# Kernel optimization log

Measured on AMD Instinct MI355X. Metric: run time of the kernel, lower is better.

## Reference

```python
import jax, jax.numpy as jnp
import numpy as np

NUM_BINS = 8
C_OUT = 64
CA_RED = 8  # channel-attention reduction (CBAM default-style)


def _bn(x, g, b):
    # BatchNorm1d in training mode: batch statistics, eps=1e-3
    mu = x.mean(0)
    var = x.var(0)
    return (x - mu) / jnp.sqrt(var + 1e-3) * g + b


def setup_inputs() -> dict:
    key = jax.random.key(0)
    ks = jax.random.split(key, 20)
    Nv, U = 400000, 200000
    s = 0.05
    inp = {
        'voxel_features': jax.random.normal(ks[0], (Nv, 5), jnp.float32),
        'voxel_features_coords': jax.random.randint(ks[1], (Nv, 4), 0, NUM_BINS),
        'v_feat_unq_coords': jax.random.randint(ks[2], (U,), 0, 1000000),
        'v_feat_unq_inv': jax.random.randint(ks[3], (Nv,), 0, U),
        'v_feat_unq_cnt': jax.random.randint(ks[4], (U,), 0, 5),
        # up_dimension: Linear(5,32)+ReLU, Linear(32,64)
        'up_w1': jax.random.normal(ks[5], (5, C_OUT // 2), jnp.float32) * s,
        'up_b1': jnp.zeros((C_OUT // 2,), jnp.float32),
        'up_w2': jax.random.normal(ks[6], (C_OUT // 2, C_OUT), jnp.float32) * s,
        'up_b2': jnp.zeros((C_OUT,), jnp.float32),
        # ZBAM (CBAM-1d): channel-attention shared MLP + spatial conv k=7
        'ca_w1': jax.random.normal(ks[7], (C_OUT, C_OUT // CA_RED), jnp.float32) * s,
        'ca_w2': jax.random.normal(ks[8], (C_OUT // CA_RED, C_OUT), jnp.float32) * s,
        'sa_conv': jax.random.normal(ks[9], (1, 2, 7), jnp.float32) * s,  # OIH
        # bin_shuffle: Linear(512,256,no bias)+BN+ReLU, Linear(256,64,no bias)+BN+ReLU
        'bs_w1': jax.random.normal(ks[10], (C_OUT * NUM_BINS, C_OUT * NUM_BINS // 2), jnp.float32) * s,
        'bn1_g': jnp.ones((C_OUT * NUM_BINS // 2,), jnp.float32),
        'bn1_b': jnp.zeros((C_OUT * NUM_BINS // 2,), jnp.float32),
        'bs_w2': jax.random.normal(ks[11], (C_OUT * NUM_BINS // 2, C_OUT), jnp.float32) * s,
        'bn2_g': jnp.ones((C_OUT,), jnp.float32),
        'bn2_b': jnp.zeros((C_OUT,), jnp.float32),
    }
    return inp


def reference(voxel_features, voxel_features_coords, v_feat_unq_coords,
              v_feat_unq_inv, v_feat_unq_cnt,
              up_w1, up_b1, up_w2, up_b2,
              ca_w1, ca_w2, sa_conv,
              bs_w1, bn1_g, bn1_b, bs_w2, bn2_g, bn2_b):
    coords = voxel_features_coords
    U = v_feat_unq_coords.shape[0]
    binz = coords[:, 1]
    # --- binning: scatter voxels into (pillar, z-bin) slots ---
    src = jnp.zeros((U, NUM_BINS, 6), jnp.float32)
    src = src.at[v_feat_unq_inv, binz, 1:].set(voxel_features)
    src = src.at[:, :, 0].set(-1.0)
    src = src.at[v_feat_unq_inv, binz, 0].set(coords[:, 0].astype(jnp.float32))
    # --- occupancy mask + compaction (eager nonzero) ---
    idx = jnp.nonzero(v_feat_unq_cnt >= 2)[0]
    src = src[idx]                      # (N, P=8, 6)
    feat = src[:, :, 1:]                # (N, 8, 5)
    # --- up_dimension MLP ---
    h = jnp.maximum(feat @ up_w1 + up_b1, 0.0) @ up_w2 + up_b2  # (N, 8, 64)
    x = jnp.swapaxes(h, 1, 2)           # (N, C=64, P=8)
    # --- ZBAM: CBAM-style channel + spatial attention over z-bins ---
    def ca_mlp(v):
        return jnp.maximum(v @ ca_w1, 0.0) @ ca_w2
    ca = jax.nn.sigmoid(ca_mlp(x.mean(-1)) + ca_mlp(x.max(-1)))  # (N, C)
    x = x * ca[:, :, None]
    sa_in = jnp.stack([x.mean(1), x.max(1)], axis=1)             # (N, 2, P)
    sa = jax.lax.conv_general_dilated(sa_in, sa_conv, (1,), [(3, 3)],
                                      dimension_numbers=('NCH', 'OIH', 'NCH'))
    x = x * jax.nn.sigmoid(sa)          # (N, C, P)
    # --- bin_shuffle: flatten (C,P) row-major as torch .view does ---
    flat = x.reshape(x.shape[0], C_OUT * NUM_BINS)  # (N, 512)
    y = jnp.maximum(_bn(flat @ bs_w1, bn1_g, bn1_b), 0.0)
    y = jnp.maximum(_bn(y @ bs_w2, bn2_g, bn2_b), 0.0)
    return y
```

## Files before the change

kernel.cpp:

```cpp
#include <hip/hip_runtime.h>
#include <cmath>

typedef __attribute__((ext_vector_type(8))) short short8;
typedef __attribute__((ext_vector_type(4))) float f32x4;

__device__ __forceinline__ ushort f2b(float x) {
    union { float f; unsigned u; } v; v.f = x;
    unsigned r = v.u + 0x7FFFu + ((v.u >> 16) & 1u);
    return (ushort)(r >> 16);
}
__device__ __forceinline__ float b2f(ushort h) {
    union { unsigned u; float f; } v; v.u = ((unsigned)h) << 16; return v.f;
}
__device__ __forceinline__ float sigm(float x) { return 1.0f / (1.0f + __expf(-x)); }

template <int C>
__device__ __forceinline__ float dppf(float x) {
    return __builtin_bit_cast(float,
        __builtin_amdgcn_update_dpp(0, __builtin_bit_cast(int, x), C, 0xf, 0xf, true));
}
__device__ __forceinline__ float rsum16(float v) {
    v += dppf<0x140>(v);
    v += dppf<0x141>(v);
    v += dppf<0x1B>(v);
    v += dppf<0xB1>(v);
    return v;
}
__device__ __forceinline__ float rmax16(float v) {
    v = fmaxf(v, dppf<0x140>(v));
    v = fmaxf(v, dppf<0x141>(v));
    v = fmaxf(v, dppf<0x1B>(v));
    v = fmaxf(v, dppf<0xB1>(v));
    return v;
}
__device__ __forceinline__ float swzf16(float x) {
    return __builtin_bit_cast(float,
        __builtin_amdgcn_ds_swizzle(__builtin_bit_cast(int, x), 0x401F));
}
__device__ __forceinline__ unsigned swzu16(unsigned x) {
    return (unsigned)__builtin_amdgcn_ds_swizzle((int)x, 0x401F);
}

#define GL16(g, s) __builtin_amdgcn_global_load_lds( \
    (const __attribute__((address_space(1))) unsigned int*)(g), \
    (__attribute__((address_space(3))) unsigned int*)(s), 16, 0, 0)

__global__ void k_scatter_winner(const int* __restrict__ inv,
                                 const int* __restrict__ coords,
                                 int Nv, int* __restrict__ winner) {
    int v = blockIdx.x * 256 + threadIdx.x;
    if (v < Nv) {
        int u = inv[v];
        int b = coords[v * 4 + 1];
        atomicMax(&winner[u * 8 + b], v);
    }
}

__global__ void k_count(const int* __restrict__ cnt, int U, int* __restrict__ bc) {
    int i = blockIdx.x * 256 + threadIdx.x;
    int s = (i < U && cnt[i] >= 2) ? 1 : 0;
    unsigned long long m = __ballot(s);
    __shared__ int wc[4];
    int lane = threadIdx.x & 63, w = threadIdx.x >> 6;
    if (lane == 0) wc[w] = __popcll(m);
    __syncthreads();
    if (threadIdx.x == 0) bc[blockIdx.x] = wc[0] + wc[1] + wc[2] + wc[3];
}

__global__ void k_scan_wave(int* __restrict__ d, int n) {
    int l = threadIdx.x;
    int carry = 0;
    for (int base = 0; base < n; base += 64) {
        int v = (base + l < n) ? d[base + l] : 0;
        int s = v;
        #pragma unroll
        for (int o = 1; o < 64; o <<= 1) {
            int q = __shfl_up(s, o);
            if (l >= o) s += q;
        }
        if (base + l < n) d[base + l] = carry + s - v;
        carry += __shfl(s, 63);
    }
}

__global__ void k_write_sel(const int* __restrict__ cnt, int U,
                            const int* __restrict__ boff, int* __restrict__ sel) {
    int i = blockIdx.x * 256 + threadIdx.x;
    int s = (i < U && cnt[i] >= 2) ? 1 : 0;
    unsigned long long m = __ballot(s);
    __shared__ int wc[4];
    int lane = threadIdx.x & 63, w = threadIdx.x >> 6;
    if (lane == 0) wc[w] = __popcll(m);
    __syncthreads();
    int off = boff[blockIdx.x];
    for (int j = 0; j < w; j++) off += wc[j];
    if (s) sel[off + __popcll(m & ((1ull << lane) - 1ull))] = i;
}

__global__ void k_prep_w(const float* __restrict__ w1, const float* __restrict__ w2,
                         ushort* __restrict__ w1t, ushort* __restrict__ w2t) {
    int i = blockIdx.x * 256 + threadIdx.x;
    if (i < 512 * 256) {
        int n = i >> 9, k = i & 511;
        w1t[i] = f2b(w1[k * 256 + n]);
    }
    int j = i - 512 * 256;
    if (j >= 0 && j < 256 * 64) {
        int n = j >> 8, k = j & 255;
        w2t[j] = f2b(w2[k * 64 + n]);
    }
}

__global__ __launch_bounds__(64) void k_feat4(
    const float* __restrict__ vf, const int* __restrict__ winner,
    const int* __restrict__ sel,
    const float* __restrict__ up_w1, const float* __restrict__ up_b1,
    const float* __restrict__ up_w2, const float* __restrict__ up_b2,
    const float* __restrict__ ca_w1, const float* __restrict__ ca_w2,
    const float* __restrict__ sa_conv,
    ushort* __restrict__ xsg, int M, int nw)
{
    __shared__ float sfeat[16 * 12];

    const int l   = threadIdx.x;
    const int lr  = l & 15;
    const int lk8 = (l >> 4) * 8;
    const int qsel = (l >> 4) & 1;
    const int rowh = l >> 5;

    float w1v[5][8], b1v[8];
    #pragma unroll
    for (int p = 0; p < 5; p++)
        #pragma unroll
        for (int kk = 0; kk < 8; kk++) w1v[p][kk] = up_w1[p * 32 + lk8 + kk];
    #pragma unroll
    for (int kk = 0; kk < 8; kk++) b1v[kk] = up_b1[lk8 + kk];

    short8 bv[4];
    #pragma unroll
    for (int j = 0; j < 4; j++)
        #pragma unroll
        for (int kk = 0; kk < 8; kk++)
            bv[j][kk] = (short)f2b(up_w2[(lk8 + kk) * 64 + 16 * j + lr]);

    float b2v[4];
    #pragma unroll
    for (int j = 0; j < 4; j++) b2v[j] = up_b2[16 * j + lr];

    const int jjb = qsel * 4;
    float caw1v[4][4];
    #pragma unroll
    for (int j = 0; j < 4; j++)
        #pragma unroll
        for (int o = 0; o < 4; o++)
            caw1v[j][o] = ca_w1[(16 * j + lr) * 8 + jjb + o];
    float caw2v[4][8];
    #pragma unroll
    for (int j = 0; j < 4; j++)
        #pragma unroll
        for (int jj = 0; jj < 8; jj++)
            caw2v[j][jj] = ca_w2[jj * 64 + 16 * j + lr];
    float sas[14];
    #pragma unroll
    for (int k = 0; k < 14; k++) sas[k] = sa_conv[k];

    auto prefetch = [&](int mb, float4& o4, float& o5) {
        int wv = -1;
        if (l < 16) {
            int mm = mb + (l >> 3);
            if (mm < M) wv = winner[sel[mm] * 8 + (l & 7)];
        }
        int wl = __shfl(wv, lr);
        float4 t4 = make_float4(0.f, 0.f, 0.f, 0.f);
        float t5 = 0.f;
        if (wl >= 0) {
            if (l < 16) {
                const float* p = &vf[(size_t)wl * 5];
                t4.x = p[0]; t4.y = p[1]; t4.z = p[2]; t4.w = p[3];
            } else if (l < 32) {
                t5 = vf[(size_t)wl * 5 + 4];
            }
        }
        o4 = t4; o5 = t5;
    };

    const int step = nw * 2;
    int m2 = blockIdx.x * 2;
    float4 pf; float pf5;
    prefetch(m2, pf, pf5);

    for (; m2 < M; m2 += step) {
        if (l < 16) *(float4*)&sfeat[lr * 12] = pf;
        else if (l < 32) sfeat[(l & 15) * 12 + 4] = pf5;
        __syncthreads();
        const float4 ff = *(const float4*)&sfeat[lr * 12];
        const float f4e = sfeat[lr * 12 + 4];
        prefetch(m2 + step, pf, pf5);

        float h[8];
        #pragma unroll
        for (int kk = 0; kk < 8; kk++) {
            float a = b1v[kk];
            a = fmaf(ff.x, w1v[0][kk], a);
            a = fmaf(ff.y, w1v[1][kk], a);
            a = fmaf(ff.z, w1v[2][kk], a);
            a = fmaf(ff.w, w1v[3][kk], a);
            a = fmaf(f4e,  w1v[4][kk], a);
            h[kk] = fmaxf(a, 0.0f);
        }
        short8 af;
        #pragma unroll
        for (int kk = 0; kk < 8; kk++) af[kk] = (short)f2b(h[kk]);

        const f32x4 z = {0.f, 0.f, 0.f, 0.f};
        float x[4][4];
        #pragma unroll
        for (int j = 0; j < 4; j++) {
            f32x4 a = __builtin_amdgcn_mfma_f32_16x16x32_bf16(af, bv[j], z, 0, 0, 0);
            #pragma unroll
            for (int q = 0; q < 4; q++) x[j][q] = a[q] + b2v[j];
        }

        float cm[4], cx[4];
        #pragma unroll
        for (int j = 0; j < 4; j++) {
            float s = (x[j][0] + x[j][1]) + (x[j][2] + x[j][3]);
            float mx = fmaxf(fmaxf(x[j][0], x[j][1]), fmaxf(x[j][2], x[j][3]));
            cm[j] = (s + swzf16(s)) * 0.125f;
            cx[j] = fmaxf(mx, swzf16(mx));
        }
        float pm[4], px[4];
        #pragma unroll
        for (int o = 0; o < 4; o++) {
            float a = 0.f, b = 0.f;
            #pragma unroll
            for (int j = 0; j < 4; j++) {
                a = fmaf(cm[j], caw1v[j][o], a);
                b = fmaf(cx[j], caw1v[j][o], b);
            }
            pm[o] = a; px[o] = b;
        }
        float hso[4], hsx[4];
        #pragma unroll
        for (int o = 0; o < 4; o++) {
            float a = rsum16(pm[o]);
            float b = rsum16(px[o]);
            hso[o] = fmaxf(a, 0.f) + fmaxf(b, 0.f);
        }
        #pragma unroll
        for (int o = 0; o < 4; o++) hsx[o] = swzf16(hso[o]);
        float hs[8];
        #pragma unroll
        for (int jj = 0; jj < 8; jj++)
            hs[jj] = ((jj >> 2) == qsel) ? hso[jj & 3] : hsx[jj & 3];
        #pragma unroll
        for (int j = 0; j < 4; j++) {
            float a = 0.f;
            #pragma unroll
            for (int jj = 0; jj < 8; jj++) a = fmaf(hs[jj], caw2v[j][jj], a);
            float cv = sigm(a);
            x[j][0] *= cv; x[j][1] *= cv; x[j][2] *= cv; x[j][3] *= cv;
        }

        float sq[4], mq[4];
        #pragma unroll
        for (int q = 0; q < 4; q++) {
            float s = (x[0][q] + x[1][q]) + (x[2][q] + x[3][q]);
            float mx = fmaxf(fmaxf(x[0][q], x[1][q]), fmaxf(x[2][q], x[3][q]));
            sq[q] = rsum16(s);
            mq[q] = rmax16(mx);
        }
        float sq2[4], mq2[4];
        #pragma unroll
        for (int q = 0; q < 4; q++) { sq2[q] = swzf16(sq[q]); mq2[q] = swzf16(mq[q]); }
        float am[8], ax[8];
        #pragma unroll
        for (int b = 0; b < 8; b++) {
            int q = b & 3;
            bool own = ((b >> 2) == qsel);
            am[b] = (own ? sq[q] : sq2[q]) * (1.0f / 64.0f);
            ax[b] = own ? mq[q] : mq2[q];
        }
        float sg[8];
        #pragma unroll
        for (int b = 0; b < 8; b++) {
            float a = 0.f;
            #pragma unroll
            for (int k = 0; k < 7; k++) {
                const int p = b + k - 3;
                if (p >= 0 && p < 8) {
                    a = fmaf(am[p], sas[k], a);
                    a = fmaf(ax[p], sas[7 + k], a);
                }
            }
            sg[b] = sigm(a);
        }
        #pragma unroll
        for (int q = 0; q < 4; q++) {
            float g = qsel ? sg[4 + q] : sg[q];
            x[0][q] *= g; x[1][q] *= g; x[2][q] *= g; x[3][q] *= g;
        }

        unsigned u0[4], u1[4];
        #pragma unroll
        for (int j = 0; j < 4; j++) {
            u0[j] = (unsigned)f2b(x[j][0]) | ((unsigned)f2b(x[j][1]) << 16);
            u1[j] = (unsigned)f2b(x[j][2]) | ((unsigned)f2b(x[j][3]) << 16);
        }
        unsigned o0[4], o1[4];
        #pragma unroll
        for (int j = 0; j < 4; j++) { o0[j] = swzu16(u0[j]); o1[j] = swzu16(u1[j]); }
        if (qsel == 0 && (m2 + rowh) < M) {
            size_t base = (size_t)(m2 + rowh) * 512;
            #pragma unroll
            for (int j = 0; j < 4; j++) {
                uint4 W = make_uint4(u0[j], u1[j], o0[j], o1[j]);
                *(uint4*)&xsg[base + (16 * j + lr) * 8] = W;
            }
        }
        __syncthreads();
    }
}

__global__ __launch_bounds__(256) void k_gemm1(
    const ushort* __restrict__ A, const ushort* __restrict__ B,
    ushort* __restrict__ C, float* __restrict__ ss, int Mp)
{
    __shared__ ushort As[128 * 64];
    __shared__ ushort Bs[128 * 64];
    int t = threadIdx.x;
    int m0 = (blockIdx.x >> 1) * 128;
    int n0 = (blockIdx.x & 1) * 128;
    int l = t & 63, w = t >> 6;
    int wr = w >> 1, wc = w & 1;
    int lr = l & 15, lg = l >> 4, lk = lg * 8;
    f32x4 acc[4][4];
    #pragma unroll
    for (int i = 0; i < 4; i++)
        #pragma unroll
        for (int j = 0; j < 4; j++) acc[i][j] = (f32x4){0.f, 0.f, 0.f, 0.f};

    for (int kt = 0; kt < 512; kt += 64) {
        __syncthreads();
        #pragma unroll
        for (int q = 0; q < 4; q++) {
            int idx = q * 256 + t;
            int row = idx >> 3, kc = (idx & 7) * 8;
            int skc = kc ^ ((row & 7) << 3);
            GL16(&A[(size_t)(m0 + row) * 512 + kt + skc], &As[idx * 8]);
            GL16(&B[(size_t)(n0 + row) * 512 + kt + skc], &Bs[idx * 8]);
        }
        __syncthreads();
        #pragma unroll
        for (int s = 0; s < 2; s++) {
            short8 av[4], bvv[4];
            #pragma unroll
            for (int i = 0; i < 4; i++) {
                int row = wr * 64 + i * 16 + lr;
                av[i] = *(short8*)&As[row * 64 + ((s * 32 + lk) ^ ((row & 7) << 3))];
            }
            #pragma unroll
            for (int j = 0; j < 4; j++) {
                int row = wc * 64 + j * 16 + lr;
                bvv[j] = *(short8*)&Bs[row * 64 + ((s * 32 + lk) ^ ((row & 7) << 3))];
            }
            #pragma unroll
            for (int i = 0; i < 4; i++)
                #pragma unroll
                for (int j = 0; j < 4; j++)
                    acc[i][j] = __builtin_amdgcn_mfma_f32_16x16x32_bf16(av[i], bvv[j], acc[i][j], 0, 0, 0);
        }
    }
    int orow = m0 + wr * 64 + lg * 4;
    int ocol = n0 + wc * 64 + lr;
    float csum[4], csq[4];
    #pragma unroll
    for (int j = 0; j < 4; j++) { csum[j] = 0.f; csq[j] = 0.f; }
    #pragma unroll
    for (int i = 0; i < 4; i++)
        #pragma unroll
        for (int j = 0; j < 4; j++)
            #pragma unroll
            for (int q = 0; q < 4; q++) {
                float v = acc[i][j][q];
                C[(size_t)(orow + i * 16 + q) * 256 + ocol + j * 16] = f2b(v);
                csum[j] += v; csq[j] += v * v;
            }
    #pragma unroll
    for (int j = 0; j < 4; j++) {
        csum[j] += __shfl_xor(csum[j], 16); csum[j] += __shfl_xor(csum[j], 32);
        csq[j]  += __shfl_xor(csq[j], 16);  csq[j]  += __shfl_xor(csq[j], 32);
    }
    if (l < 16) {
        #pragma unroll
        for (int j = 0; j < 4; j++) {
            atomicAdd(&ss[ocol + j * 16], csum[j]);
            atomicAdd(&ss[256 + ocol + j * 16], csq[j]);
        }
    }
}

__global__ void k_finalize(const float* __restrict__ ss, const float* __restrict__ g,
                           const float* __restrict__ b, int C, float invM,
                           float* __restrict__ scsh) {
    int c = threadIdx.x;
    if (c < C) {
        float mean = ss[c] * invM;
        float var  = ss[C + c] * invM - mean * mean;
        float inv  = rsqrtf(var + 0.001f);
        float sc   = g[c] * inv;
        scsh[c]     = sc;
        scsh[C + c] = b[c] - mean * sc;
    }
}

__global__ __launch_bounds__(256) void k_gemm2(
    const ushort* __restrict__ A, const ushort* __restrict__ B,
    const float* __restrict__ scsh1,
    float* __restrict__ out, float* __restrict__ ss2, int M)
{
    __shared__ ushort As[128 * 64];
    __shared__ ushort Bs[64 * 64];
    __shared__ float s1[512];
    int t = threadIdx.x;
    for (int i = t; i < 512; i += 256) s1[i] = scsh1[i];
    int m0 = blockIdx.x * 128;
    int l = t & 63, w = t >> 6;
    int wr = w >> 1, wc = w & 1;
    int lr = l & 15, lg = l >> 4, lk = lg * 8;
    f32x4 acc[4][2];
    #pragma unroll
    for (int i = 0; i < 4; i++)
        #pragma unroll
        for (int j = 0; j < 2; j++) acc[i][j] = (f32x4){0.f, 0.f, 0.f, 0.f};

    for (int kt = 0; kt < 256; kt += 64) {
        __syncthreads();
        #pragma unroll
        for (int q = 0; q < 2; q++) {
            int idx = q * 256 + t;
            int row = idx >> 3, kc = (idx & 7) * 8;
            int skc = kc ^ ((row & 7) << 3);
            GL16(&B[(size_t)row * 256 + kt + skc], &Bs[idx * 8]);
        }
        #pragma unroll
        for (int q = 0; q < 4; q++) {
            int idx = q * 256 + t;
            int row = idx >> 3, kc = (idx & 7) * 8;
            uint4 av = *(const uint4*)&A[(size_t)(m0 + row) * 256 + kt + kc];
            ushort* ap = (ushort*)&av;
            uint4 pk;
            unsigned* pkp = (unsigned*)&pk;
            #pragma unroll
            for (int h = 0; h < 4; h++) {
                int k0 = kt + kc + 2 * h;
                float v0 = fmaxf(fmaf(b2f(ap[2*h]),   s1[k0],   s1[256 + k0]),   0.f);
                float v1 = fmaxf(fmaf(b2f(ap[2*h+1]), s1[k0+1], s1[256 + k0+1]), 0.f);
                pkp[h] = (unsigned)f2b(v0) | ((unsigned)f2b(v1) << 16);
            }
            *(uint4*)&As[row * 64 + (kc ^ ((row & 7) << 3))] = pk;
        }
        __syncthreads();
        #pragma unroll
        for (int s = 0; s < 2; s++) {
            short8 av[4], bvv[2];
            #pragma unroll
            for (int i = 0; i < 4; i++) {
                int row = wr * 64 + i * 16 + lr;
                av[i] = *(short8*)&As[row * 64 + ((s * 32 + lk) ^ ((row & 7) << 3))];
            }
            #pragma unroll
            for (int j = 0; j < 2; j++) {
                int row = wc * 32 + j * 16 + lr;
                bvv[j] = *(short8*)&Bs[row * 64 + ((s * 32 + lk) ^ ((row & 7) << 3))];
            }
            #pragma unroll
            for (int i = 0; i < 4; i++)
                #pragma unroll
                for (int j = 0; j < 2; j++)
                    acc[i][j] = __builtin_amdgcn_mfma_f32_16x16x32_bf16(av[i], bvv[j], acc[i][j], 0, 0, 0);
        }
    }
    int orow = m0 + wr * 64 + lg * 4;
    int ocol = wc * 32 + lr;
    float csum[2], csq[2];
    #pragma unroll
    for (int j = 0; j < 2; j++) { csum[j] = 0.f; csq[j] = 0.f; }
    #pragma unroll
    for (int i = 0; i < 4; i++)
        #pragma unroll
        for (int j = 0; j < 2; j++)
            #pragma unroll
            for (int q = 0; q < 4; q++) {
                int rr = orow + i * 16 + q;
                if (rr < M) {
                    float v = acc[i][j][q];
                    out[(size_t)rr * 64 + ocol + j * 16] = v;
                    csum[j] += v; csq[j] += v * v;
                }
            }
    #pragma unroll
    for (int j = 0; j < 2; j++) {
        csum[j] += __shfl_xor(csum[j], 16); csum[j] += __shfl_xor(csum[j], 32);
        csq[j]  += __shfl_xor(csq[j], 16);  csq[j]  += __shfl_xor(csq[j], 32);
    }
    if (l < 16) {
        #pragma unroll
        for (int j = 0; j < 2; j++) {
            atomicAdd(&ss2[ocol + j * 16], csum[j]);
            atomicAdd(&ss2[64 + ocol + j * 16], csq[j]);
        }
    }
}

__global__ void k_bn2_apply4(float4* __restrict__ out4, const float* __restrict__ scsh2, int n4) {
    int i = blockIdx.x * 256 + threadIdx.x;
    if (i < n4) {
        float4 v = out4[i];
        int c0 = (i & 15) * 4;
        v.x = fmaxf(fmaf(v.x, scsh2[c0 + 0], scsh2[64 + c0 + 0]), 0.f);
        v.y = fmaxf(fmaf(v.y, scsh2[c0 + 1], scsh2[64 + c0 + 1]), 0.f);
        v.z = fmaxf(fmaf(v.z, scsh2[c0 + 2], scsh2[64 + c0 + 2]), 0.f);
        v.w = fmaxf(fmaf(v.w, scsh2[c0 + 3], scsh2[64 + c0 + 3]), 0.f);
        out4[i] = v;
    }
}

extern "C" void kernel_launch(void* const* d_in, const int* in_sizes, int n_in,
                              void* d_out, int out_size, void* d_ws, size_t ws_size,
                              hipStream_t stream) {
    const float* vf     = (const float*)d_in[0];
    const int*   coords = (const int*)d_in[1];
    const int*   inv    = (const int*)d_in[3];
    const int*   cnt    = (const int*)d_in[4];
    const float* up_w1  = (const float*)d_in[5];
    const float* up_b1  = (const float*)d_in[6];
    const float* up_w2  = (const float*)d_in[7];
    const float* up_b2  = (const float*)d_in[8];
    const float* ca_w1  = (const float*)d_in[9];
    const float* ca_w2  = (const float*)d_in[10];
    const float* sa_conv= (const float*)d_in[11];
    const float* bs_w1  = (const float*)d_in[12];
    const float* bn1_g  = (const float*)d_in[13];
    const float* bn1_b  = (const float*)d_in[14];
    const float* bs_w2  = (const float*)d_in[15];
    const float* bn2_g  = (const float*)d_in[16];
    const float* bn2_b  = (const float*)d_in[17];

    int Nv = in_sizes[3];
    int U  = in_sizes[4];
    int M  = out_size / 64;
    int Mp = (M + 127) & ~127;
    float* out = (float*)d_out;

    char* ws = (char*)d_ws;
    auto alloc = [&](size_t bytes) -> char* {
        char* p = ws;
        ws += (bytes + 255) / 256 * 256;
        return p;
    };
    int nb = (U + 255) / 256;
    int*    winner = (int*)alloc((size_t)U * 8 * 4);
    int*    bc     = (int*)alloc((size_t)nb * 4);
    int*    sel    = (int*)alloc((size_t)M * 4);
    float*  ss     = (float*)alloc(640 * 4);
    float*  scsh1  = (float*)alloc(512 * 4);
    float*  scsh2  = (float*)alloc(128 * 4);
    ushort* w1t    = (ushort*)alloc((size_t)512 * 256 * 2);
    ushort* w2t    = (ushort*)alloc((size_t)256 * 64 * 2);
    ushort* xsg    = (ushort*)alloc((size_t)Mp * 512 * 2);
    ushort* y1     = (ushort*)alloc((size_t)Mp * 256 * 2);

    hipMemsetAsync(winner, 0xFF, (size_t)U * 8 * 4, stream);
    hipMemsetAsync(ss, 0, 640 * 4, stream);
    if (Mp > M)
        hipMemsetAsync(xsg + (size_t)M * 512, 0, (size_t)(Mp - M) * 512 * 2, stream);

    k_prep_w<<<(512 * 256 + 256 * 64 + 255) / 256, 256, 0, stream>>>(bs_w1, bs_w2, w1t, w2t);
    k_scatter_winner<<<(Nv + 255) / 256, 256, 0, stream>>>(inv, coords, Nv, winner);
    k_count<<<nb, 256, 0, stream>>>(cnt, U, bc);
    k_scan_wave<<<1, 64, 0, stream>>>(bc, nb);
    k_write_sel<<<nb, 256, 0, stream>>>(cnt, U, bc, sel);

    int nwf = 2048;
    k_feat4<<<nwf, 64, 0, stream>>>(
        vf, winner, sel, up_w1, up_b1, up_w2, up_b2,
        ca_w1, ca_w2, sa_conv, xsg, M, nwf);

    k_gemm1<<<(Mp / 128) * 2, 256, 0, stream>>>(xsg, w1t, y1, ss, Mp);
    k_finalize<<<1, 256, 0, stream>>>(ss, bn1_g, bn1_b, 256, 1.0f / (float)M, scsh1);

    k_gemm2<<<Mp / 128, 256, 0, stream>>>(y1, w2t, scsh1, out, ss + 512, M);
    k_finalize<<<1, 64, 0, stream>>>(ss + 512, bn2_g, bn2_b, 64, 1.0f / (float)M, scsh2);

    int n4 = (M * 64) / 4;
    k_bn2_apply4<<<(n4 + 255) / 256, 256, 0, stream>>>((float4*)out, scsh2, n4);
}
```

Measured before the change: 415.2 us.

## Merge prologue kernels, fold scan and BN finalize into consumers, drop memsets

Merges the winner scatter, block counting, weight transpose/bf16 conversion and stats zeroing into one prologue kernel. The single-wave scan is removed by having each write_sel block sum the preceding block counts itself. The two BN finalize kernels are folded into gemm2 and the BN2 apply kernel, and the padding memset is replaced by zero-writes inside k_feat4, whose grid is raised from 2048 to 8192 blocks. The aim is to cut launch count and serial tiny kernels, at the cost of redundant prefix summation (quadratic in block count) and repeated per-block BN stat computation.

```diff
diff --git a/kernel.cpp b/kernel.cpp
--- a/kernel.cpp
+++ b/kernel.cpp
@@ -45,61 +45,29 @@
     (const __attribute__((address_space(1))) unsigned int*)(g), \
     (__attribute__((address_space(3))) unsigned int*)(s), 16, 0, 0)
 
-__global__ void k_scatter_winner(const int* __restrict__ inv,
-                                 const int* __restrict__ coords,
-                                 int Nv, int* __restrict__ winner) {
-    int v = blockIdx.x * 256 + threadIdx.x;
-    if (v < Nv) {
-        int u = inv[v];
-        int b = coords[v * 4 + 1];
-        atomicMax(&winner[u * 8 + b], v);
-    }
-}
-
-__global__ void k_count(const int* __restrict__ cnt, int U, int* __restrict__ bc) {
+__global__ __launch_bounds__(256) void k_prologue(
+    const int* __restrict__ inv, const int* __restrict__ coords, int Nv,
+    const int* __restrict__ cnt, int U, int* __restrict__ bc, int nbc,
+    const float* __restrict__ w1, const float* __restrict__ w2,
+    ushort* __restrict__ w1t, ushort* __restrict__ w2t,
+    float* __restrict__ ss, int* __restrict__ winner)
+{
     int i = blockIdx.x * 256 + threadIdx.x;
-    int s = (i < U && cnt[i] >= 2) ? 1 : 0;
-    unsigned long long m = __ballot(s);
-    __shared__ int wc[4];
-    int lane = threadIdx.x & 63, w = threadIdx.x >> 6;
-    if (lane == 0) wc[w] = __popcll(m);
-    __syncthreads();
-    if (threadIdx.x == 0) bc[blockIdx.x] = wc[0] + wc[1] + wc[2] + wc[3];
-}
-
-__global__ void k_scan_wave(int* __restrict__ d, int n) {
-    int l = threadIdx.x;
-    int carry = 0;
-    for (int base = 0; base < n; base += 64) {
-        int v = (base + l < n) ? d[base + l] : 0;
-        int s = v;
-        #pragma unroll
-        for (int o = 1; o < 64; o <<= 1) {
-            int q = __shfl_up(s, o);
-            if (l >= o) s += q;
-        }
-        if (base + l < n) d[base + l] = carry + s - v;
-        carry += __shfl(s, 63);
-    }
-}
-
-__global__ void k_write_sel(const int* __restrict__ cnt, int U,
-                            const int* __restrict__ boff, int* __restrict__ sel) {
-    int i = blockIdx.x * 256 + threadIdx.x;
-    int s = (i < U && cnt[i] >= 2) ? 1 : 0;
-    unsigned long long m = __ballot(s);
-    __shared__ int wc[4];
-    int lane = threadIdx.x & 63, w = threadIdx.x >> 6;
-    if (lane == 0) wc[w] = __popcll(m);
-    __syncthreads();
-    int off = boff[blockIdx.x];
-    for (int j = 0; j < w; j++) off += wc[j];
-    if (s) sel[off + __popcll(m & ((1ull << lane) - 1ull))] = i;
-}
-
-__global__ void k_prep_w(const float* __restrict__ w1, const float* __restrict__ w2,
-                         ushort* __restrict__ w1t, ushort* __restrict__ w2t) {
-    int i = blockIdx.x * 256 + threadIdx.x;
+    if (i < Nv) {
+        int u = inv[i];
+        int b = coords[i * 4 + 1];
+        atomicMax(&winner[u * 8 + b], i);
+    }
+    {
+        int s = (i < U && cnt[i] >= 2) ? 1 : 0;
+        unsigned long long m = __ballot(s);
+        __shared__ int wc[4];
+        int lane = threadIdx.x & 63, w = threadIdx.x >> 6;
+        if (lane == 0) wc[w] = __popcll(m);
+        __syncthreads();
+        if (threadIdx.x == 0 && blockIdx.x < nbc)
+            bc[blockIdx.x] = wc[0] + wc[1] + wc[2] + wc[3];
+    }
     if (i < 512 * 256) {
         int n = i >> 9, k = i & 511;
         w1t[i] = f2b(w1[k * 256 + n]);
@@ -109,6 +77,28 @@
         int n = j >> 8, k = j & 255;
         w2t[j] = f2b(w2[k * 64 + n]);
     }
+    if (i < 640) ss[i] = 0.0f;
+}
+
+__global__ __launch_bounds__(256) void k_write_sel(
+    const int* __restrict__ cnt, int U,
+    const int* __restrict__ bc, int* __restrict__ sel)
+{
+    int i = blockIdx.x * 256 + threadIdx.x;
+    int s = (i < U && cnt[i] >= 2) ? 1 : 0;
+    unsigned long long m = __ballot(s);
+    __shared__ int wc[4], wsum[4];
+    int lane = threadIdx.x & 63, w = threadIdx.x >> 6;
+    if (lane == 0) wc[w] = __popcll(m);
+    int part = 0;
+    for (int b = threadIdx.x; b < blockIdx.x; b += 256) part += bc[b];
+    #pragma unroll
+    for (int o = 1; o < 64; o <<= 1) part += __shfl_xor(part, o);
+    if (lane == 0) wsum[w] = part;
+    __syncthreads();
+    int off = wsum[0] + wsum[1] + wsum[2] + wsum[3];
+    for (int jj = 0; jj < w; jj++) off += wc[jj];
+    if (s) sel[off + __popcll(m & ((1ull << lane) - 1ull))] = i;
 }
 
 __global__ __launch_bounds__(64) void k_feat4(
@@ -118,7 +108,7 @@
     const float* __restrict__ up_w2, const float* __restrict__ up_b2,
     const float* __restrict__ ca_w1, const float* __restrict__ ca_w2,
     const float* __restrict__ sa_conv,
-    ushort* __restrict__ xsg, int M, int nw)
+    ushort* __restrict__ xsg, int M, int Mp, int nw)
 {
     __shared__ float sfeat[16 * 12];
 
@@ -189,7 +179,7 @@
     float4 pf; float pf5;
     prefetch(m2, pf, pf5);
 
-    for (; m2 < M; m2 += step) {
+    for (; m2 < Mp; m2 += step) {
         if (l < 16) *(float4*)&sfeat[lr * 12] = pf;
         else if (l < 32) sfeat[(l & 15) * 12 + 4] = pf5;
         __syncthreads();
@@ -310,12 +300,20 @@
         unsigned o0[4], o1[4];
         #pragma unroll
         for (int j = 0; j < 4; j++) { o0[j] = swzu16(u0[j]); o1[j] = swzu16(u1[j]); }
-        if (qsel == 0 && (m2 + rowh) < M) {
-            size_t base = (size_t)(m2 + rowh) * 512;
-            #pragma unroll
-            for (int j = 0; j < 4; j++) {
-                uint4 W = make_uint4(u0[j], u1[j], o0[j], o1[j]);
-                *(uint4*)&xsg[base + (16 * j + lr) * 8] = W;
+        int mrow = m2 + rowh;
+        if (qsel == 0 && mrow < Mp) {
+            size_t base = (size_t)mrow * 512;
+            if (mrow < M) {
+                #pragma unroll
+                for (int j = 0; j < 4; j++) {
+                    uint4 W = make_uint4(u0[j], u1[j], o0[j], o1[j]);
+                    *(uint4*)&xsg[base + (16 * j + lr) * 8] = W;
+                }
+            } else {
+                const uint4 Z = make_uint4(0u, 0u, 0u, 0u);
+                #pragma unroll
+                for (int j = 0; j < 4; j++)
+                    *(uint4*)&xsg[base + (16 * j + lr) * 8] = Z;
             }
         }
         __syncthreads();
@@ -400,30 +398,23 @@
     }
 }
 
-__global__ void k_finalize(const float* __restrict__ ss, const float* __restrict__ g,
-                           const float* __restrict__ b, int C, float invM,
-                           float* __restrict__ scsh) {
-    int c = threadIdx.x;
-    if (c < C) {
-        float mean = ss[c] * invM;
-        float var  = ss[C + c] * invM - mean * mean;
-        float inv  = rsqrtf(var + 0.001f);
-        float sc   = g[c] * inv;
-        scsh[c]     = sc;
-        scsh[C + c] = b[c] - mean * sc;
-    }
-}
-
 __global__ __launch_bounds__(256) void k_gemm2(
     const ushort* __restrict__ A, const ushort* __restrict__ B,
-    const float* __restrict__ scsh1,
+    const float* __restrict__ ss, const float* __restrict__ bn1_g,
+    const float* __restrict__ bn1_b, float invM,
     float* __restrict__ out, float* __restrict__ ss2, int M)
 {
     __shared__ ushort As[128 * 64];
     __shared__ ushort Bs[64 * 64];
     __shared__ float s1[512];
     int t = threadIdx.x;
-    for (int i = t; i < 512; i += 256) s1[i] = scsh1[i];
+    {
+        float mean = ss[t] * invM;
+        float var  = ss[256 + t] * invM - mean * mean;
+        float sc   = bn1_g[t] * rsqrtf(var + 0.001f);
+        s1[t]       = sc;
+        s1[256 + t] = bn1_b[t] - mean * sc;
+    }
     int m0 = blockIdx.x * 128;
     int l = t & 63, w = t >> 6;
     int wr = w >> 1, wc = w & 1;
@@ -513,15 +504,29 @@
     }
 }
 
-__global__ void k_bn2_apply4(float4* __restrict__ out4, const float* __restrict__ scsh2, int n4) {
+__global__ __launch_bounds__(256) void k_bn2_apply4(
+    float4* __restrict__ out4, const float* __restrict__ ss2,
+    const float* __restrict__ bn2_g, const float* __restrict__ bn2_b,
+    float invM, int n4)
+{
+    __shared__ float s2[128];
+    if (threadIdx.x < 64) {
+        int c = threadIdx.x;
+        float mean = ss2[c] * invM;
+        float var  = ss2[64 + c] * invM - mean * mean;
+        float sc   = bn2_g[c] * rsqrtf(var + 0.001f);
+        s2[c]      = sc;
+        s2[64 + c] = bn2_b[c] - mean * sc;
+    }
+    __syncthreads();
     int i = blockIdx.x * 256 + threadIdx.x;
     if (i < n4) {
         float4 v = out4[i];
         int c0 = (i & 15) * 4;
-        v.x = fmaxf(fmaf(v.x, scsh2[c0 + 0], scsh2[64 + c0 + 0]), 0.f);
-        v.y = fmaxf(fmaf(v.y, scsh2[c0 + 1], scsh2[64 + c0 + 1]), 0.f);
-        v.z = fmaxf(fmaf(v.z, scsh2[c0 + 2], scsh2[64 + c0 + 2]), 0.f);
-        v.w = fmaxf(fmaf(v.w, scsh2[c0 + 3], scsh2[64 + c0 + 3]), 0.f);
+        v.x = fmaxf(fmaf(v.x, s2[c0 + 0], s2[64 + c0 + 0]), 0.f);
+        v.y = fmaxf(fmaf(v.y, s2[c0 + 1], s2[64 + c0 + 1]), 0.f);
+        v.z = fmaxf(fmaf(v.z, s2[c0 + 2], s2[64 + c0 + 2]), 0.f);
+        v.w = fmaxf(fmaf(v.w, s2[c0 + 3], s2[64 + c0 + 3]), 0.f);
         out4[i] = v;
     }
 }
@@ -564,35 +569,29 @@
     int*    bc     = (int*)alloc((size_t)nb * 4);
     int*    sel    = (int*)alloc((size_t)M * 4);
     float*  ss     = (float*)alloc(640 * 4);
-    float*  scsh1  = (float*)alloc(512 * 4);
-    float*  scsh2  = (float*)alloc(128 * 4);
     ushort* w1t    = (ushort*)alloc((size_t)512 * 256 * 2);
     ushort* w2t    = (ushort*)alloc((size_t)256 * 64 * 2);
     ushort* xsg    = (ushort*)alloc((size_t)Mp * 512 * 2);
     ushort* y1     = (ushort*)alloc((size_t)Mp * 256 * 2);
 
     hipMemsetAsync(winner, 0xFF, (size_t)U * 8 * 4, stream);
-    hipMemsetAsync(ss, 0, 640 * 4, stream);
-    if (Mp > M)
-        hipMemsetAsync(xsg + (size_t)M * 512, 0, (size_t)(Mp - M) * 512 * 2, stream);
-
-    k_prep_w<<<(512 * 256 + 256 * 64 + 255) / 256, 256, 0, stream>>>(bs_w1, bs_w2, w1t, w2t);
-    k_scatter_winner<<<(Nv + 255) / 256, 256, 0, stream>>>(inv, coords, Nv, winner);
-    k_count<<<nb, 256, 0, stream>>>(cnt, U, bc);
-    k_scan_wave<<<1, 64, 0, stream>>>(bc, nb);
+
+    int npro = (Nv + 255) / 256;
+    k_prologue<<<npro, 256, 0, stream>>>(inv, coords, Nv, cnt, U, bc, nb,
+                                         bs_w1, bs_w2, w1t, w2t, ss, winner);
     k_write_sel<<<nb, 256, 0, stream>>>(cnt, U, bc, sel);
 
-    int nwf = 2048;
+    int nwf = 8192;
     k_feat4<<<nwf, 64, 0, stream>>>(
         vf, winner, sel, up_w1, up_b1, up_w2, up_b2,
-        ca_w1, ca_w2, sa_conv, xsg, M, nwf);
+        ca_w1, ca_w2, sa_conv, xsg, M, Mp, nwf);
 
     k_gemm1<<<(Mp / 128) * 2, 256, 0, stream>>>(xsg, w1t, y1, ss, Mp);
-    k_finalize<<<1, 256, 0, stream>>>(ss, bn1_g, bn1_b, 256, 1.0f / (float)M, scsh1);
-
-    k_gemm2<<<Mp / 128, 256, 0, stream>>>(y1, w2t, scsh1, out, ss + 512, M);
-    k_finalize<<<1, 64, 0, stream>>>(ss + 512, bn2_g, bn2_b, 64, 1.0f / (float)M, scsh2);
+
+    k_gemm2<<<Mp / 128, 256, 0, stream>>>(y1, w2t, ss, bn1_g, bn1_b,
+                                          1.0f / (float)M, out, ss + 512, M);
 
     int n4 = (M * 64) / 4;
-    k_bn2_apply4<<<(n4 + 255) / 256, 256, 0, stream>>>((float4*)out, scsh2, n4);
-}
+    k_bn2_apply4<<<(n4 + 255) / 256, 256, 0, stream>>>(
+        (float4*)out, ss + 512, bn2_g, bn2_b, 1.0f / (float)M, n4);
+}
```

After: 386.8 us. 1.07x faster.
